# Performance work log

Hardware: AMD Instinct MI355X
Metric: run time of the kernel (lower is better)

Reference implementation:

```python
import jax, jax.numpy as jnp
import numpy as np
from jax import lax


def _prelu(x, a):
    return jnp.where(x >= 0, x, a * x)


def _conv1d(x, w):
    # x: (B, 1, L), w: (rank, 1, 3) -> (B, rank, L), padding=1
    return lax.conv_general_dilated(x, w, window_strides=(1,), padding='SAME',
                                    dimension_numbers=('NCH', 'OIH', 'NCH'))


def setup_inputs() -> dict:
    key = jax.random.key(0)
    ks = jax.random.split(key, 8)
    B, C, H, W, R = 32, 256, 56, 56, 64
    return {
        'x': jax.random.normal(ks[0], (B, C, H, W), dtype=jnp.float32),
        'Wc': jax.random.normal(ks[1], (R, 1, 3), dtype=jnp.float32) * 0.1,
        'ac': jnp.float32(0.25),
        'Ww': jax.random.normal(ks[2], (R, 1, 3), dtype=jnp.float32) * 0.1,
        'aw': jnp.float32(0.25),
        'Wh': jax.random.normal(ks[3], (R, 1, 3), dtype=jnp.float32) * 0.1,
        'ah': jnp.float32(0.25),
        'W3d': jax.random.normal(ks[4], (1, 1, 3, 3, 3), dtype=jnp.float32) * 0.1,
    }


def reference(x, Wc, ac, Ww, aw, Wh, ah, W3d):
    # x: (B, C, H, W)
    # channel branch: GAP over HW -> conv1d over channel axis
    gap_c = jnp.mean(x, axis=(2, 3))[:, None, :]            # (B, 1, C)
    c_out = _prelu(_conv1d(gap_c, Wc), ac)                  # (B, R, C)
    c_out = jnp.swapaxes(c_out, 1, 2)                       # (B, C, R)
    # width branch: mean over C then H -> conv1d over W
    gap_w = jnp.mean(x, axis=1, keepdims=True).mean(axis=2) # (B, 1, W)
    w_out = _prelu(_conv1d(gap_w, Ww), aw)                  # (B, R, W)
    # height branch: mean over C then W -> conv1d over H
    gap_h = jnp.mean(x, axis=1, keepdims=True).mean(axis=3) # (B, 1, H)
    h_out = _prelu(_conv1d(gap_h, Wh), ah)                  # (B, R, H)
    # CP reconstruction: outer product over (H, W), then contract rank with channel factors
    nrhw = jnp.einsum('brh,brw->brhw', h_out, w_out)        # (B, R, H, W)
    nchw = jnp.einsum('bcr,brhw->bchw', c_out, nrhw)        # (B, C, H, W)
    gcrw = jax.nn.softmax(nchw, axis=1)                     # softmax over channels
    # conv3d gated residual
    res = lax.conv_general_dilated(x[:, None], W3d, window_strides=(1, 1, 1),
                                   padding='SAME',
                                   dimension_numbers=('NCDHW', 'OIDHW', 'NCDHW'))[:, 0]
    return res * gcrw + x
```

## Files before the change

### kernel.cpp

```cpp
#include <hip/hip_runtime.h>
#include <hip/hip_bf16.h>

typedef float f32x4 __attribute__((ext_vector_type(4)));
typedef float f32x2 __attribute__((ext_vector_type(2)));
typedef short s16x8 __attribute__((ext_vector_type(8)));
typedef unsigned short ush4 __attribute__((ext_vector_type(4)));
typedef unsigned u32x4 __attribute__((ext_vector_type(4)));
typedef unsigned u32x2 __attribute__((ext_vector_type(2)));

#define B_ 32
#define C_ 256
#define H_ 56
#define W_ 56
#define HW_ (H_*W_)
#define CH_ 14336
#define NHT 28
#define CPH 68
#define SGPT 260
#define CGRP 16

#define OFF_SG0T  0
#define OFF_SCOUT 29120
#define OFF_SWOUT 63936
#define OFF_SRED0 63936
#define OFF_SRED1 68032
#define OFF_SHOUT 72640
#define SMEM_SZ   73184

__device__ __forceinline__ unsigned short f2bf(float f) {
    unsigned u = __float_as_uint(f);
    u += 0x7fffu + ((u >> 16) & 1u);
    return (unsigned short)(u >> 16);
}
__device__ __forceinline__ float bf2f(unsigned short u) {
    return __uint_as_float((unsigned)u << 16);
}
__device__ __forceinline__ f32x4 bf2f4(ush4 u) {
    f32x4 r; r[0] = bf2f(u[0]); r[1] = bf2f(u[1]); r[2] = bf2f(u[2]); r[3] = bf2f(u[3]);
    return r;
}
__device__ __forceinline__ unsigned pkbf(float lo, float hi) {
    __hip_bfloat162 h = __float22bfloat162_rn(make_float2(lo, hi));
    unsigned r;
    __builtin_memcpy(&r, &h, 4);
    return r;
}
__device__ __forceinline__ s16x8 pack8(f32x4 a, f32x4 b) {
    u32x4 t = { pkbf(a[0], a[1]), pkbf(a[2], a[3]), pkbf(b[0], b[1]), pkbf(b[2], b[3]) };
    s16x8 r;
    __builtin_memcpy(&r, &t, 16);
    return r;
}
__device__ __forceinline__ s16x8 cat8(ush4 a, ush4 b) {
    s16x8 r;
    r[0] = (short)a[0]; r[1] = (short)a[1]; r[2] = (short)a[2]; r[3] = (short)a[3];
    r[4] = (short)b[0]; r[5] = (short)b[1]; r[6] = (short)b[2]; r[7] = (short)b[3];
    return r;
}
__device__ __forceinline__ float dpp_shr1(float v) {
    return __int_as_float(__builtin_amdgcn_mov_dpp(__float_as_int(v), 0x138, 0xf, 0xf, true));
}
__device__ __forceinline__ float dpp_shl1(float v) {
    return __int_as_float(__builtin_amdgcn_mov_dpp(__float_as_int(v), 0x130, 0xf, 0xf, true));
}

__global__ __launch_bounds__(832) void k_reduce(const float* __restrict__ x,
                                                float* __restrict__ gapc,
                                                float* __restrict__ gw,
                                                float* __restrict__ gh) {
    __shared__ float chanpart[13 * CGRP];
    __shared__ float rowsum[H_];
    __shared__ float colsum[W_];
    const int bid = blockIdx.x;
    const int b  = bid >> 4;
    const int c0 = (bid & 15) * CGRP;
    const int tid = threadIdx.x;
    const int lane = tid & 63, wid = tid >> 6;
    if (tid < H_) rowsum[tid] = 0.f;
    else if (tid >= 64 && tid < 64 + W_) colsum[tid - 64] = 0.f;
    __syncthreads();

    const bool act = tid < 784;
    const int j = act ? tid : 0;
    const float* px = x + (size_t)(b * C_ + c0) * HW_ + j * 4;
    f32x4 posacc = {0, 0, 0, 0};
    #pragma unroll 4
    for (int c = 0; c < CGRP; ++c) {
        f32x4 v = {0, 0, 0, 0};
        if (act) v = *(const f32x4*)(px + (size_t)c * HW_);
        posacc += v;
        float s = v[0] + v[1] + v[2] + v[3];
        #pragma unroll
        for (int d = 1; d < 64; d <<= 1) s += __shfl_xor(s, d, 64);
        if (lane == 0) chanpart[wid * CGRP + c] = s;
    }
    if (act) {
        const int h = j / 14, w4 = j % 14;
        atomicAdd(&rowsum[h], posacc[0] + posacc[1] + posacc[2] + posacc[3]);
        atomicAdd(&colsum[w4 * 4 + 0], posacc[0]);
        atomicAdd(&colsum[w4 * 4 + 1], posacc[1]);
        atomicAdd(&colsum[w4 * 4 + 2], posacc[2]);
        atomicAdd(&colsum[w4 * 4 + 3], posacc[3]);
    }
    __syncthreads();
    if (tid < CGRP) {
        float t = 0.f;
        #pragma unroll
        for (int w = 0; w < 13; ++w) t += chanpart[w * CGRP + tid];
        gapc[b * C_ + c0 + tid] = t * (1.f / HW_);
    } else if (tid >= 64 && tid < 64 + H_) {
        atomicAdd(&gh[b * H_ + (tid - 64)], rowsum[tid - 64]);
    } else if (tid >= 128 && tid < 128 + W_) {
        atomicAdd(&gw[b * W_ + (tid - 128)], colsum[tid - 128]);
    }
}

template<bool EDGE>
__device__ __forceinline__ void conv_store(
    const float* __restrict__ xb, const float* __restrict__ W3,
    const unsigned short* sg0, const unsigned short* sg1,
    float invS0, float invS1, int h0, int cbase, int lane, int lw,
    float* __restrict__ outb)
{
    #pragma unroll 1
    for (int q = 0; q < 4; ++q) {
        const int c4 = cbase + q * 4;
        f32x2 res01[4] = {{0,0},{0,0},{0,0},{0,0}};
        float xm0[4], xm1[4];
        #pragma unroll
        for (int ci = 0; ci < 6; ++ci) {
            const int cc  = c4 - 1 + ci;
            const bool cok = (cc >= 0) && (cc < C_);
            const int ccl = cc < 0 ? 0 : (cc > C_ - 1 ? C_ - 1 : cc);
            const float* pc = xb + (size_t)ccl * HW_ + lw;
            #pragma unroll
            for (int jr = 0; jr < 4; ++jr) {
                float v;
                bool keep = cok && (lane < W_);
                if (EDGE) {
                    const int hh  = h0 - 1 + jr;
                    keep = keep && (hh >= 0) && (hh < H_);
                    const int hcl = hh < 0 ? 0 : (hh > H_ - 1 ? H_ - 1 : hh);
                    v = pc[hcl * W_];
                } else {
                    v = pc[(h0 - 1 + jr) * W_];
                }
                v = keep ? v : 0.f;
                if (ci >= 1 && ci <= 4) {
                    if (jr == 1) xm0[ci - 1] = v;
                    if (jr == 2) xm1[ci - 1] = v;
                }
                const float vl = dpp_shr1(v);
                const float vr = dpp_shl1(v);
                #pragma unroll
                for (int kl = 0; kl < 4; ++kl) {
                    const int dz = ci - kl;
                    if (dz >= 0 && dz <= 2) {
                        if (jr >= 1 && jr <= 2) {
                            const int wi0 = (dz * 3 + jr) * 3;
                            const int wi1 = (dz * 3 + jr - 1) * 3;
                            const f32x2 vl2 = {vl, vl}, v2 = {v, v}, vr2 = {vr, vr};
                            const f32x2 w0 = {W3[wi0+0], W3[wi1+0]};
                            const f32x2 w1 = {W3[wi0+1], W3[wi1+1]};
                            const f32x2 w2 = {W3[wi0+2], W3[wi1+2]};
                            res01[kl] = __builtin_elementwise_fma(w0, vl2,
                                        __builtin_elementwise_fma(w1, v2,
                                        __builtin_elementwise_fma(w2, vr2, res01[kl])));
                        } else if (jr == 0) {
                            const int wi = (dz * 3 + 0) * 3;
                            res01[kl][0] = fmaf(W3[wi], vl, fmaf(W3[wi+1], v, fmaf(W3[wi+2], vr, res01[kl][0])));
                        } else {
                            const int wi = (dz * 3 + 2) * 3;
                            res01[kl][1] = fmaf(W3[wi], vl, fmaf(W3[wi+1], v, fmaf(W3[wi+2], vr, res01[kl][1])));
                        }
                    }
                }
            }
        }
        if (lane < W_) {
            const ush4 q0 = *(const ush4*)&sg0[lane * SGPT + c4];
            const ush4 q1 = *(const ush4*)&sg1[lane * SGPT + c4];
            #pragma unroll
            for (int kk = 0; kk < 4; ++kk) {
                const int c = c4 + kk;
                const size_t xi = ((size_t)c * H_ + h0) * W_ + lane;
                outb[xi]      = fmaf(res01[kk][0], bf2f(q0[kk]) * invS0, xm0[kk]);
                outb[xi + W_] = fmaf(res01[kk][1], bf2f(q1[kk]) * invS1, xm1[kk]);
            }
        }
    }
}

__global__ __launch_bounds__(1024)
void k_main(
    const float* __restrict__ x,
    const float* __restrict__ Wc, const float* __restrict__ acp,
    const float* __restrict__ Ww, const float* __restrict__ awp,
    const float* __restrict__ Wh, const float* __restrict__ ahp,
    const float* __restrict__ W3,
    const float* __restrict__ gapc, const float* __restrict__ gw,
    const float* __restrict__ gh,
    float* __restrict__ out)
{
    __shared__ __align__(16) char smem[SMEM_SZ];
    unsigned short* sg0   = (unsigned short*)(smem + OFF_SG0T);
    unsigned short* scout = (unsigned short*)(smem + OFF_SCOUT);
    unsigned short* sg1   = scout;
    unsigned short* swout = (unsigned short*)(smem + OFF_SWOUT);
    float* sred0 = (float*)(smem + OFF_SRED0);
    float* sred1 = (float*)(smem + OFF_SRED1);
    float* shout = (float*)(smem + OFF_SHOUT);

    const int bid  = blockIdx.x;
    const int slot = bid >> 3;
    const int b    = (bid & 7) * 4 + slot / NHT;
    const int h0   = (slot % NHT) * 2;

    const int tid  = threadIdx.x;
    const int lane = tid & 63;
    const int wid  = tid >> 6;
    const int g    = lane >> 4;
    const int col  = lane & 15;
    const int lw   = (lane < W_) ? lane : (W_ - 1);
    const float ac = acp[0], aw = awp[0], ah = ahp[0];

    {
        const float* gc = gapc + b * C_;
        const int c  = tid >> 2;
        const int rq = tid & 3;
        const float gm = (c >= 1)      ? gc[c - 1] : 0.f;
        const float g0 = gc[c];
        const float gp = (c < C_ - 1)  ? gc[c + 1] : 0.f;
        const float* wc = Wc + rq * 48;
        unsigned short* dst = &scout[c * CPH + rq * 16];
        #pragma unroll
        for (int i = 0; i < 16; i += 4) {
            f32x4 vv;
            #pragma unroll
            for (int k = 0; k < 4; ++k) {
                float v = wc[(i+k)*3+0] * gm + wc[(i+k)*3+1] * g0 + wc[(i+k)*3+2] * gp;
                vv[k] = (v >= 0.f) ? v : ac * v;
            }
            u32x2 pkd = { pkbf(vv[0], vv[1]), pkbf(vv[2], vv[3]) };
            *(u32x2*)&dst[i] = pkd;
        }
    }
    {
        const float* gwb = gw + b * W_;
        const int w  = tid >> 4;
        const int rq = tid & 15;
        float gm = 0.f, g0 = 0.f, gp = 0.f;
        if (w < W_) {
            gm = (w >= 1)     ? gwb[w - 1] * (1.f / CH_) : 0.f;
            g0 = gwb[w] * (1.f / CH_);
            gp = (w < W_ - 1) ? gwb[w + 1] * (1.f / CH_) : 0.f;
        }
        const float* ww = Ww + rq * 12;
        f32x4 vv;
        #pragma unroll
        for (int k = 0; k < 4; ++k) {
            float v = ww[k*3+0] * gm + ww[k*3+1] * g0 + ww[k*3+2] * gp;
            vv[k] = (v >= 0.f) ? v : aw * v;
        }
        u32x2 pkd = { pkbf(vv[0], vv[1]), pkbf(vv[2], vv[3]) };
        *(u32x2*)&swout[w * CPH + rq * 4] = pkd;
    }
    if (tid < 2 * 64) {
        const float* ghb = gh + b * H_;
        const int hr = tid >> 6, r = tid & 63;
        const int h = h0 + hr;
        const float gm = (h >= 1)     ? ghb[h - 1] * (1.f / CH_) : 0.f;
        const float g0 = ghb[h] * (1.f / CH_);
        const float gp = (h < H_ - 1) ? ghb[h + 1] * (1.f / CH_) : 0.f;
        float v = Wh[r * 3 + 0] * gm + Wh[r * 3 + 1] * g0 + Wh[r * 3 + 2] * gp;
        shout[hr * CPH + r] = (v >= 0.f) ? v : ah * v;
    }
    __syncthreads();

    const int cbase = wid * 16;
    const int crow  = cbase + col;
    const int cr    = cbase + g * 4;

    f32x4 acc[8];
    #pragma unroll
    for (int t = 0; t < 8; ++t) acc[t] = (f32x4){0,0,0,0};
    #pragma unroll
    for (int kc = 0; kc < 2; ++kc) {
        const int r0 = kc * 32 + g * 4;
        f32x4 ca = bf2f4(*(ush4*)&scout[crow * CPH + r0]);
        f32x4 cb = bf2f4(*(ush4*)&scout[crow * CPH + r0 + 16]);
        f32x4 ha0 = *(f32x4*)&shout[0 * CPH + r0];
        f32x4 hb0 = *(f32x4*)&shout[0 * CPH + r0 + 16];
        f32x4 ha1 = *(f32x4*)&shout[1 * CPH + r0];
        f32x4 hb1 = *(f32x4*)&shout[1 * CPH + r0 + 16];
        s16x8 af0 = pack8(ca * ha0, cb * hb0);
        s16x8 af1 = pack8(ca * ha1, cb * hb1);
        #pragma unroll
        for (int t = 0; t < 4; ++t) {
            s16x8 bfr = cat8(*(ush4*)&swout[(t*16+col)*CPH + r0],
                             *(ush4*)&swout[(t*16+col)*CPH + r0 + 16]);
            acc[t]     = __builtin_amdgcn_mfma_f32_16x16x32_bf16(af0, bfr, acc[t],     0, 0, 0);
            acc[4 + t] = __builtin_amdgcn_mfma_f32_16x16x32_bf16(af1, bfr, acc[4 + t], 0, 0, 0);
        }
    }
    float s0p, s1p;
    {
        float st0[4], st1[4];
        #pragma unroll
        for (int t = 0; t < 4; ++t) {
            #pragma unroll
            for (int j = 0; j < 4; ++j) { acc[t][j] = __expf(acc[t][j]); acc[4+t][j] = __expf(acc[4+t][j]); }
            float s0 = acc[t][0] + acc[t][1] + acc[t][2] + acc[t][3];
            float s1 = acc[4+t][0] + acc[4+t][1] + acc[4+t][2] + acc[4+t][3];
            s0 += __shfl_xor(s0, 16, 64);  s0 += __shfl_xor(s0, 32, 64);
            s1 += __shfl_xor(s1, 16, 64);  s1 += __shfl_xor(s1, 32, 64);
            st0[t] = s0; st1[t] = s1;
        }
        s0p = (g == 0) ? st0[0] : (g == 1) ? st0[1] : (g == 2) ? st0[2] : st0[3];
        s1p = (g == 0) ? st1[0] : (g == 1) ? st1[1] : (g == 2) ? st1[2] : st1[3];
        #pragma unroll
        for (int t = 0; t < 4; ++t) {
            const int w = t * 16 + col;
            if (w < W_) {
                u32x2 pkd = { pkbf(acc[t][0], acc[t][1]), pkbf(acc[t][2], acc[t][3]) };
                *(u32x2*)&sg0[w * SGPT + cr] = pkd;
            }
        }
    }
    __syncthreads();
    {
        #pragma unroll
        for (int t = 0; t < 4; ++t) {
            const int w = t * 16 + col;
            if (w < W_) {
                u32x2 pkd = { pkbf(acc[4+t][0], acc[4+t][1]), pkbf(acc[4+t][2], acc[4+t][3]) };
                *(u32x2*)&sg1[w * SGPT + cr] = pkd;
            }
        }
        sred0[wid * 64 + lane] = s0p;
        sred1[wid * 64 + lane] = s1p;
    }
    __syncthreads();

    float invS0, invS1;
    {
        float T0 = 0.f, T1 = 0.f;
        #pragma unroll
        for (int t = 0; t < 16; ++t) {
            T0 += sred0[t * 64 + lane];
            T1 += sred1[t * 64 + lane];
        }
        invS0 = 1.f / T0;
        invS1 = 1.f / T1;
    }

    const float* xb = x + (size_t)b * C_ * HW_;
    float* outb = out + (size_t)b * C_ * HW_;
    if (h0 == 0 || h0 == H_ - 2)
        conv_store<true >(xb, W3, sg0, sg1, invS0, invS1, h0, cbase, lane, lw, outb);
    else
        conv_store<false>(xb, W3, sg0, sg1, invS0, invS1, h0, cbase, lane, lw, outb);
}

extern "C" void kernel_launch(void* const* d_in, const int* in_sizes, int n_in,
                              void* d_out, int out_size, void* d_ws, size_t ws_size,
                              hipStream_t stream) {
    const float* x  = (const float*)d_in[0];
    const float* Wc = (const float*)d_in[1];
    const float* ac = (const float*)d_in[2];
    const float* Ww = (const float*)d_in[3];
    const float* aw = (const float*)d_in[4];
    const float* Wh = (const float*)d_in[5];
    const float* ah = (const float*)d_in[6];
    const float* W3 = (const float*)d_in[7];
    float* out  = (float*)d_out;
    float* gapc = (float*)d_ws;
    float* gwp  = gapc + B_ * C_;
    float* ghp  = gwp + B_ * W_;

    (void)hipMemsetAsync(gwp, 0, (size_t)(B_ * W_ + B_ * H_) * sizeof(float), stream);
    k_reduce<<<dim3(B_ * (C_ / CGRP)), dim3(832), 0, stream>>>(x, gapc, gwp, ghp);
    k_main<<<dim3(B_ * NHT), dim3(1024), 0, stream>>>(
        x, Wc, ac, Ww, aw, Wh, ah, W3, gapc, gwp, ghp, out);
}
```

Baseline: 108.5 us.

## Remap conv stage to 4-wide W vectors per lane with channel-major gate layout

Changes the conv3d/output stage so each lane handles 4 consecutive W positions for one channel (14 lanes per channel, 4 channels per wave) using float4 loads and stores, instead of one W position across 4 channels with scalar accesses. The softmax gate buffers become channel-major (stride 60) so the epilogue reads 4 contiguous bf16 values, and the per-W inverse sums move to shared memory behind an extra barrier. The intent is fewer global memory instructions and no redundant reloads of neighbouring channels. In exchange the gate writes become scattered 16-bit stores, 8 of 64 lanes sit idle, and the neighbour values across 4-wide groups need masked DPP shifts.

```diff
diff --git a/kernel.cpp b/kernel.cpp
--- a/kernel.cpp
+++ b/kernel.cpp
@@ -16,16 +16,18 @@
 #define CH_ 14336
 #define NHT 28
 #define CPH 68
-#define SGPT 260
+#define SGP2 60
 #define CGRP 16
 
-#define OFF_SG0T  0
-#define OFF_SCOUT 29120
-#define OFF_SWOUT 63936
-#define OFF_SRED0 63936
-#define OFF_SRED1 68032
-#define OFF_SHOUT 72640
-#define SMEM_SZ   73184
+#define OFF_SG0   0
+#define OFF_SCOUT 30720
+#define OFF_SWOUT 65536
+#define OFF_SRED0 65536
+#define OFF_SRED1 69632
+#define OFF_SHOUT 74240
+#define OFF_SINV0 74784
+#define OFF_SINV1 75040
+#define SMEM_SZ   75296
 
 __device__ __forceinline__ unsigned short f2bf(float f) {
     unsigned u = __float_as_uint(f);
@@ -119,74 +121,90 @@
 __device__ __forceinline__ void conv_store(
     const float* __restrict__ xb, const float* __restrict__ W3,
     const unsigned short* sg0, const unsigned short* sg1,
-    float invS0, float invS1, int h0, int cbase, int lane, int lw,
+    const float* __restrict__ sinv0, const float* __restrict__ sinv1,
+    int h0, int cbase, int lane,
     float* __restrict__ outb)
 {
+    const int cg = lane / 14;
+    const int wq = lane - cg * 14;
+    const bool active = lane < 56;
+    const int cgc = (cg < 4) ? cg : 3;
+    const int w0 = wq * 4;
+
     #pragma unroll 1
     for (int q = 0; q < 4; ++q) {
-        const int c4 = cbase + q * 4;
-        f32x2 res01[4] = {{0,0},{0,0},{0,0},{0,0}};
-        float xm0[4], xm1[4];
-        #pragma unroll
-        for (int ci = 0; ci < 6; ++ci) {
-            const int cc  = c4 - 1 + ci;
-            const bool cok = (cc >= 0) && (cc < C_);
+        const int c = cbase + q * 4 + cgc;
+        f32x2 racc[4] = {{0,0},{0,0},{0,0},{0,0}};
+        f32x4 xm0, xm1;
+        #pragma unroll
+        for (int dz = 0; dz < 3; ++dz) {
+            const int cc = c + dz - 1;
+            const bool cok = (cc >= 0) && (cc < C_) && active;
             const int ccl = cc < 0 ? 0 : (cc > C_ - 1 ? C_ - 1 : cc);
-            const float* pc = xb + (size_t)ccl * HW_ + lw;
+            const float* pc = xb + (size_t)ccl * HW_ + w0;
             #pragma unroll
             for (int jr = 0; jr < 4; ++jr) {
-                float v;
-                bool keep = cok && (lane < W_);
+                f32x4 v;
+                bool keep = cok;
                 if (EDGE) {
-                    const int hh  = h0 - 1 + jr;
+                    const int hh = h0 - 1 + jr;
                     keep = keep && (hh >= 0) && (hh < H_);
                     const int hcl = hh < 0 ? 0 : (hh > H_ - 1 ? H_ - 1 : hh);
-                    v = pc[hcl * W_];
+                    v = *(const f32x4*)(pc + hcl * W_);
                 } else {
-                    v = pc[(h0 - 1 + jr) * W_];
+                    v = *(const f32x4*)(pc + (h0 - 1 + jr) * W_);
                 }
-                v = keep ? v : 0.f;
-                if (ci >= 1 && ci <= 4) {
-                    if (jr == 1) xm0[ci - 1] = v;
-                    if (jr == 2) xm1[ci - 1] = v;
-                }
-                const float vl = dpp_shr1(v);
-                const float vr = dpp_shl1(v);
-                #pragma unroll
-                for (int kl = 0; kl < 4; ++kl) {
-                    const int dz = ci - kl;
-                    if (dz >= 0 && dz <= 2) {
-                        if (jr >= 1 && jr <= 2) {
-                            const int wi0 = (dz * 3 + jr) * 3;
-                            const int wi1 = (dz * 3 + jr - 1) * 3;
-                            const f32x2 vl2 = {vl, vl}, v2 = {v, v}, vr2 = {vr, vr};
-                            const f32x2 w0 = {W3[wi0+0], W3[wi1+0]};
-                            const f32x2 w1 = {W3[wi0+1], W3[wi1+1]};
-                            const f32x2 w2 = {W3[wi0+2], W3[wi1+2]};
-                            res01[kl] = __builtin_elementwise_fma(w0, vl2,
-                                        __builtin_elementwise_fma(w1, v2,
-                                        __builtin_elementwise_fma(w2, vr2, res01[kl])));
-                        } else if (jr == 0) {
-                            const int wi = (dz * 3 + 0) * 3;
-                            res01[kl][0] = fmaf(W3[wi], vl, fmaf(W3[wi+1], v, fmaf(W3[wi+2], vr, res01[kl][0])));
-                        } else {
-                            const int wi = (dz * 3 + 2) * 3;
-                            res01[kl][1] = fmaf(W3[wi], vl, fmaf(W3[wi+1], v, fmaf(W3[wi+2], vr, res01[kl][1])));
-                        }
+                if (!keep) v = (f32x4){0, 0, 0, 0};
+                if (dz == 1 && jr == 1) xm0 = v;
+                if (dz == 1 && jr == 2) xm1 = v;
+                float prevw = dpp_shr1(v[3]);
+                prevw = (wq == 0) ? 0.f : prevw;
+                float nextx = dpp_shl1(v[0]);
+                nextx = (wq == 13) ? 0.f : nextx;
+                const float vls[4] = { prevw, v[0], v[1], v[2] };
+                const float vrs[4] = { v[1], v[2], v[3], nextx };
+                if (jr >= 1 && jr <= 2) {
+                    const int wi0 = (dz * 3 + jr) * 3;
+                    const int wi1 = (dz * 3 + jr - 1) * 3;
+                    const f32x2 wl = {W3[wi0+0], W3[wi1+0]};
+                    const f32x2 wc = {W3[wi0+1], W3[wi1+1]};
+                    const f32x2 wr = {W3[wi0+2], W3[wi1+2]};
+                    #pragma unroll
+                    for (int j = 0; j < 4; ++j) {
+                        const f32x2 a = {vls[j], vls[j]};
+                        const f32x2 m = {v[j], v[j]};
+                        const f32x2 z = {vrs[j], vrs[j]};
+                        racc[j] = __builtin_elementwise_fma(wl, a,
+                                  __builtin_elementwise_fma(wc, m,
+                                  __builtin_elementwise_fma(wr, z, racc[j])));
                     }
+                } else if (jr == 0) {
+                    const int wi = (dz * 3 + 0) * 3;
+                    #pragma unroll
+                    for (int j = 0; j < 4; ++j)
+                        racc[j][0] = fmaf(W3[wi], vls[j], fmaf(W3[wi+1], v[j], fmaf(W3[wi+2], vrs[j], racc[j][0])));
+                } else {
+                    const int wi = (dz * 3 + 2) * 3;
+                    #pragma unroll
+                    for (int j = 0; j < 4; ++j)
+                        racc[j][1] = fmaf(W3[wi], vls[j], fmaf(W3[wi+1], v[j], fmaf(W3[wi+2], vrs[j], racc[j][1])));
                 }
             }
         }
-        if (lane < W_) {
-            const ush4 q0 = *(const ush4*)&sg0[lane * SGPT + c4];
-            const ush4 q1 = *(const ush4*)&sg1[lane * SGPT + c4];
+        if (active) {
+            const ush4 g0 = *(const ush4*)&sg0[c * SGP2 + w0];
+            const ush4 g1 = *(const ush4*)&sg1[c * SGP2 + w0];
+            const f32x4 i0 = *(const f32x4*)&sinv0[w0];
+            const f32x4 i1 = *(const f32x4*)&sinv1[w0];
+            f32x4 o0, o1;
             #pragma unroll
-            for (int kk = 0; kk < 4; ++kk) {
-                const int c = c4 + kk;
-                const size_t xi = ((size_t)c * H_ + h0) * W_ + lane;
-                outb[xi]      = fmaf(res01[kk][0], bf2f(q0[kk]) * invS0, xm0[kk]);
-                outb[xi + W_] = fmaf(res01[kk][1], bf2f(q1[kk]) * invS1, xm1[kk]);
+            for (int j = 0; j < 4; ++j) {
+                o0[j] = fmaf(racc[j][0], bf2f(g0[j]) * i0[j], xm0[j]);
+                o1[j] = fmaf(racc[j][1], bf2f(g1[j]) * i1[j], xm1[j]);
             }
+            float* po = outb + (size_t)c * HW_ + h0 * W_ + w0;
+            *(f32x4*)po        = o0;
+            *(f32x4*)(po + W_) = o1;
         }
     }
 }
@@ -203,13 +221,15 @@
     float* __restrict__ out)
 {
     __shared__ __align__(16) char smem[SMEM_SZ];
-    unsigned short* sg0   = (unsigned short*)(smem + OFF_SG0T);
+    unsigned short* sg0   = (unsigned short*)(smem + OFF_SG0);
     unsigned short* scout = (unsigned short*)(smem + OFF_SCOUT);
     unsigned short* sg1   = scout;
     unsigned short* swout = (unsigned short*)(smem + OFF_SWOUT);
     float* sred0 = (float*)(smem + OFF_SRED0);
     float* sred1 = (float*)(smem + OFF_SRED1);
     float* shout = (float*)(smem + OFF_SHOUT);
+    float* sinv0 = (float*)(smem + OFF_SINV0);
+    float* sinv1 = (float*)(smem + OFF_SINV1);
 
     const int bid  = blockIdx.x;
     const int slot = bid >> 3;
@@ -221,7 +241,6 @@
     const int wid  = tid >> 6;
     const int g    = lane >> 4;
     const int col  = lane & 15;
-    const int lw   = (lane < W_) ? lane : (W_ - 1);
     const float ac = acp[0], aw = awp[0], ah = ahp[0];
 
     {
@@ -322,8 +341,10 @@
         for (int t = 0; t < 4; ++t) {
             const int w = t * 16 + col;
             if (w < W_) {
-                u32x2 pkd = { pkbf(acc[t][0], acc[t][1]), pkbf(acc[t][2], acc[t][3]) };
-                *(u32x2*)&sg0[w * SGPT + cr] = pkd;
+                sg0[(cr + 0) * SGP2 + w] = f2bf(acc[t][0]);
+                sg0[(cr + 1) * SGP2 + w] = f2bf(acc[t][1]);
+                sg0[(cr + 2) * SGP2 + w] = f2bf(acc[t][2]);
+                sg0[(cr + 3) * SGP2 + w] = f2bf(acc[t][3]);
             }
         }
     }
@@ -333,8 +354,10 @@
         for (int t = 0; t < 4; ++t) {
             const int w = t * 16 + col;
             if (w < W_) {
-                u32x2 pkd = { pkbf(acc[4+t][0], acc[4+t][1]), pkbf(acc[4+t][2], acc[4+t][3]) };
-                *(u32x2*)&sg1[w * SGPT + cr] = pkd;
+                sg1[(cr + 0) * SGP2 + w] = f2bf(acc[4+t][0]);
+                sg1[(cr + 1) * SGP2 + w] = f2bf(acc[4+t][1]);
+                sg1[(cr + 2) * SGP2 + w] = f2bf(acc[4+t][2]);
+                sg1[(cr + 3) * SGP2 + w] = f2bf(acc[4+t][3]);
             }
         }
         sred0[wid * 64 + lane] = s0p;
@@ -342,24 +365,24 @@
     }
     __syncthreads();
 
-    float invS0, invS1;
-    {
+    if (wid == 0 && lane < W_) {
         float T0 = 0.f, T1 = 0.f;
         #pragma unroll
         for (int t = 0; t < 16; ++t) {
             T0 += sred0[t * 64 + lane];
             T1 += sred1[t * 64 + lane];
         }
-        invS0 = 1.f / T0;
-        invS1 = 1.f / T1;
-    }
+        sinv0[lane] = 1.f / T0;
+        sinv1[lane] = 1.f / T1;
+    }
+    __syncthreads();
 
     const float* xb = x + (size_t)b * C_ * HW_;
     float* outb = out + (size_t)b * C_ * HW_;
     if (h0 == 0 || h0 == H_ - 2)
-        conv_store<true >(xb, W3, sg0, sg1, invS0, invS1, h0, cbase, lane, lw, outb);
+        conv_store<true >(xb, W3, sg0, sg1, sinv0, sinv1, h0, cbase, lane, outb);
     else
-        conv_store<false>(xb, W3, sg0, sg1, invS0, invS1, h0, cbase, lane, lw, outb);
+        conv_store<false>(xb, W3, sg0, sg1, sinv0, sinv1, h0, cbase, lane, outb);
 }
 
 extern "C" void kernel_launch(void* const* d_in, const int* in_sizes, int n_in,
```

After: 112.1 us. 3.3% more time.
